# Kernel tuning notes

Hardware: AMD Instinct MI355X
Metric: run time of the kernel (lower is better)

Reference implementation:

```python
import jax, jax.numpy as jnp
import numpy as np

N = 10000
E = 160000
IN_DIM = 256
PROJ_DIM = 512
HIDDEN = 512
OUT_DIM = 512
HEADS1, HEADS2, HEADS3 = 4, 4, 1
NEG_SLOPE = 0.2  # PyG GATConv default


def gat_conv(x, edge_index, W, att_src, att_dst, bias, heads, out_c, concat):
    """PyG GATConv (eval mode), with self-loops already appended to edge_index.
    x: [N, F_in]; W: [F_in, heads*out_c]; att_src/att_dst: [heads, out_c]; bias: [heads*out_c] or [out_c]."""
    n = x.shape[0]
    h = (x @ W).reshape(n, heads, out_c)            # [N, H, C]
    a_src = jnp.einsum('nhc,hc->nh', h, att_src)     # [N, H]
    a_dst = jnp.einsum('nhc,hc->nh', h, att_dst)     # [N, H]
    src, dst = edge_index[0], edge_index[1]
    e = jax.nn.leaky_relu(a_src[src] + a_dst[dst], NEG_SLOPE)  # [E, H]
    # segment softmax over incoming edges per destination node
    e_max = jax.ops.segment_max(e, dst, num_segments=n)
    e_exp = jnp.exp(e - e_max[dst])
    denom = jax.ops.segment_sum(e_exp, dst, num_segments=n)
    alpha = e_exp / denom[dst]                       # [E, H]
    msg = alpha[:, :, None] * h[src]                 # [E, H, C]
    out = jax.ops.segment_sum(msg, dst, num_segments=n)  # [N, H, C]
    out = out.reshape(n, heads * out_c) if concat else out.mean(axis=1)
    return out + bias


def setup_inputs() -> dict:
    key = jax.random.key(0)
    ks = jax.random.split(key, 16)
    g = 0.1
    inp = {
        'x': jax.random.normal(ks[0], (N, IN_DIM), dtype=jnp.float32),
        'edge_index': jax.random.randint(ks[1], (2, E), 0, N, dtype=jnp.int64),
        'proj_W': jax.random.normal(ks[2], (IN_DIM, PROJ_DIM), dtype=jnp.float32) * g,
        'proj_b': jnp.zeros((PROJ_DIM,), dtype=jnp.float32),
        'W1': jax.random.normal(ks[3], (PROJ_DIM, HEADS1 * HIDDEN), dtype=jnp.float32) * g,
        'as1': jax.random.normal(ks[4], (HEADS1, HIDDEN), dtype=jnp.float32) * g,
        'ad1': jax.random.normal(ks[5], (HEADS1, HIDDEN), dtype=jnp.float32) * g,
        'b1': jnp.zeros((HEADS1 * HIDDEN,), dtype=jnp.float32),
        'W2': jax.random.normal(ks[6], (HEADS1 * HIDDEN, HEADS2 * HIDDEN), dtype=jnp.float32) * g * 0.5,
        'as2': jax.random.normal(ks[7], (HEADS2, HIDDEN), dtype=jnp.float32) * g,
        'ad2': jax.random.normal(ks[8], (HEADS2, HIDDEN), dtype=jnp.float32) * g,
        'b2': jnp.zeros((HEADS2 * HIDDEN,), dtype=jnp.float32),
        'W3': jax.random.normal(ks[9], (HEADS2 * HIDDEN, HEADS3 * OUT_DIM), dtype=jnp.float32) * g * 0.5,
        'as3': jax.random.normal(ks[10], (HEADS3, OUT_DIM), dtype=jnp.float32) * g,
        'ad3': jax.random.normal(ks[11], (HEADS3, OUT_DIM), dtype=jnp.float32) * g,
        'b3': jnp.zeros((OUT_DIM,), dtype=jnp.float32),
    }
    return inp


def reference(x, edge_index, proj_W, proj_b, W1, as1, ad1, b1, W2, as2, ad2, b2, W3, as3, ad3, b3):
    # append self-loops once (PyG GATConv add_self_loops=True)
    loops = jnp.arange(N, dtype=edge_index.dtype)
    ei = jnp.concatenate([edge_index, jnp.stack([loops, loops])], axis=1)
    h = x @ proj_W + proj_b                                   # [N, 512]
    h = jax.nn.elu(gat_conv(h, ei, W1, as1, ad1, b1, HEADS1, HIDDEN, True))
    h = jax.nn.elu(gat_conv(h, ei, W2, as2, ad2, b2, HEADS2, HIDDEN, True))
    return gat_conv(h, ei, W3, as3, ad3, b3, HEADS3, OUT_DIM, False)  # [N, 512]
```

## Files before the change

kernel.cpp:

```cpp
#include <hip/hip_runtime.h>
#include <hip/hip_bf16.h>


#define LB(x) __launch_bounds__(x)

typedef unsigned short u16;
typedef unsigned int u32;
typedef __attribute__((ext_vector_type(8))) short short8;
typedef __attribute__((ext_vector_type(8))) short bf16x8;
typedef __attribute__((ext_vector_type(8))) _Float16 f16x8;
typedef __attribute__((ext_vector_type(4))) float f32x4;

__device__ __forceinline__ float b2f(u16 u) {
    union { float f; u32 u; } x;
    x.u = ((u32)u) << 16;
    return x.f;
}
__device__ __forceinline__ u16 f2b(float f) {
    u32 u = __float_as_uint(f);
    u = (u + 0x7FFFu + ((u >> 16) & 1u)) >> 16;
    return (u16)u;
}
__device__ __forceinline__ u16 f2h(float f) {
    union { _Float16 h; u16 u; } x;
    x.h = (_Float16)f;
    return x.u;
}
__device__ __forceinline__ float h2f(u16 u) {
    union { _Float16 h; u16 u; } x;
    x.u = u;
    return (float)x.h;
}
__device__ __forceinline__ void lds_cp16(const void* g, void* l) {
    __builtin_amdgcn_global_load_lds(
        (const __attribute__((address_space(1))) unsigned int*)g,
        (__attribute__((address_space(3))) unsigned int*)l, 16, 0, 0);
}

__global__ void k_deg(const int* __restrict__ ei, int E, int Np, int* __restrict__ deg) {
    int e = blockIdx.x * blockDim.x + threadIdx.x;
    if (e >= E + Np) return;
    int dst = (e < E) ? ei[E + e] : (e - E);
    atomicAdd(&deg[dst], 1);
}

__global__ LB(256) void k_s1(const int* __restrict__ deg, int* __restrict__ row_ptr,
                             int* __restrict__ bsum, int n) {
    __shared__ int sh[256];
    int b = blockIdx.x, t = threadIdx.x;
    int i = b * 256 + t;
    int v = (i < n) ? deg[i] : 0;
    sh[t] = v;
    __syncthreads();
    #pragma unroll
    for (int off = 1; off < 256; off <<= 1) {
        int add = (t >= off) ? sh[t - off] : 0;
        __syncthreads();
        sh[t] += add;
        __syncthreads();
    }
    if (i < n) row_ptr[i + 1] = sh[t];
    if (t == 255) bsum[b] = sh[255];
}

__global__ LB(64) void k_s2(int* __restrict__ bsum, int* __restrict__ boff, int nb) {
    __shared__ int sh[64];
    int t = threadIdx.x;
    sh[t] = (t < nb) ? bsum[t] : 0;
    __syncthreads();
    #pragma unroll
    for (int off = 1; off < 64; off <<= 1) {
        int add = (t >= off) ? sh[t - off] : 0;
        __syncthreads();
        sh[t] += add;
        __syncthreads();
    }
    if (t < nb) boff[t] = (t == 0) ? 0 : sh[t - 1];
}

__global__ LB(256) void k_s3(const int* __restrict__ deg, int* __restrict__ row_ptr,
                             const int* __restrict__ boff, int* __restrict__ cursor, int n) {
    int b = blockIdx.x, t = threadIdx.x;
    int i = b * 256 + t;
    if (i == 0) row_ptr[0] = 0;
    if (i < n) {
        int inc = row_ptr[i + 1] + boff[b];
        row_ptr[i + 1] = inc;
        cursor[i] = inc - deg[i];
    }
}

__global__ void k_fill(const int* __restrict__ ei, int E, int Np,
                       int* __restrict__ cursor, int* __restrict__ col_src) {
    int e = blockIdx.x * blockDim.x + threadIdx.x;
    if (e >= E + Np) return;
    int src, dst;
    if (e < E) { src = ei[e]; dst = ei[E + e]; }
    else       { src = dst = e - E; }
    int pos = atomicAdd(&cursor[dst], 1);
    col_src[pos] = src;
}

__global__ void k_pack(const float* __restrict__ in, u16* __restrict__ hi,
                       u16* __restrict__ lo, int n4) {
    int i = blockIdx.x * blockDim.x + threadIdx.x;
    if (i >= n4) return;
    float4 v = ((const float4*)in)[i];
    ushort4 h, l;
    h.x = f2b(v.x); l.x = f2b(v.x - b2f(h.x));
    h.y = f2b(v.y); l.y = f2b(v.y - b2f(h.y));
    h.z = f2b(v.z); l.z = f2b(v.z - b2f(h.z));
    h.w = f2b(v.w); l.w = f2b(v.w - b2f(h.w));
    ((ushort4*)hi)[i] = h;
    ((ushort4*)lo)[i] = l;
}

template<bool F16>
__global__ LB(256) void k_wt_pack(const float* __restrict__ W, u16* __restrict__ Whi,
                                  u16* __restrict__ Wlo, int K, int Nn) {
    __shared__ float sh[32][33];
    int n0 = blockIdx.x * 32, k0 = blockIdx.y * 32;
    int c = threadIdx.x & 31, r0 = threadIdx.x >> 5;
    #pragma unroll
    for (int r = r0; r < 32; r += 8)
        sh[r][c] = W[(size_t)(k0 + r) * Nn + n0 + c];
    __syncthreads();
    #pragma unroll
    for (int r = r0; r < 32; r += 8) {
        float v = sh[c][r];
        if (F16) {
            u16 hi = f2h(v);
            Whi[(size_t)(n0 + r) * K + k0 + c] = hi;
            Wlo[(size_t)(n0 + r) * K + k0 + c] = f2h(v - h2f(hi));
        } else {
            u16 hi = f2b(v);
            Whi[(size_t)(n0 + r) * K + k0 + c] = hi;
            Wlo[(size_t)(n0 + r) * K + k0 + c] = f2b(v - b2f(hi));
        }
    }
}

template<int NFR, int PREC, int OUTMODE, bool ATT>
__global__ LB(256) void k_gemm_pl(const u16* __restrict__ Ahi, const u16* __restrict__ Alo,
                                  const u16* __restrict__ Bhi, const u16* __restrict__ Blo,
                                  const float* __restrict__ bias,
                                  u16* __restrict__ Chi, u16* __restrict__ Clo,
                                  u16* __restrict__ Cf16,
                                  const float* __restrict__ att_s, const float* __restrict__ att_d,
                                  float* __restrict__ a_src, float* __restrict__ a_dst,
                                  int HH, int M, int K, int Nn) {
    constexpr int BN = NFR * 32;
    constexpr int ALO_SZ = (PREC == 0) ? 128 * 32 : 8;
    __shared__ u16 AsHi[128 * 32];
    __shared__ u16 AsLo[ALO_SZ];
    __shared__ u16 BsHi[BN * 32], BsLo[BN * 32];
    const int tid  = threadIdx.x;
    const int lane = tid & 63;
    const int w    = tid >> 6;
    const int wr   = w >> 1;
    const int wc   = w & 1;
    const int row0 = blockIdx.y * 128;
    const int col0 = blockIdx.x * BN;
    const int ln15 = lane & 15;
    const int lq   = lane >> 4;

    f32x4 acc[4][NFR];
    #pragma unroll
    for (int m = 0; m < 4; ++m)
        #pragma unroll
        for (int n = 0; n < NFR; ++n) acc[m][n] = (f32x4){0.f, 0.f, 0.f, 0.f};

    for (int k0 = 0; k0 < K; k0 += 32) {
        #pragma unroll
        for (int i = 0; i < 2; ++i) {
            int c = i * 256 + tid;
            int r  = 2 * (c >> 3) + (((c >> 2) ^ (c >> 4)) & 1);
            int kc = (c & 3) ^ (r & 3);
            int gra = row0 + r; if (gra >= M) gra = M - 1;
            size_t ga = (size_t)gra * K + k0 + kc * 8;
            lds_cp16(Ahi + ga, (char*)AsHi + c * 16);
            if (PREC == 0) lds_cp16(Alo + ga, (char*)AsLo + c * 16);
        }
        #pragma unroll
        for (int i = 0; i < NFR / 2; ++i) {
            int c = i * 256 + tid;
            int r  = 2 * (c >> 3) + (((c >> 2) ^ (c >> 4)) & 1);
            int kc = (c & 3) ^ (r & 3);
            size_t gb = (size_t)(col0 + r) * K + k0 + kc * 8;
            lds_cp16(Bhi + gb, (char*)BsHi + c * 16);
            lds_cp16(Blo + gb, (char*)BsLo + c * 16);
        }
        __syncthreads();
        if (PREC == 0) {
            bf16x8 ah[4], al[4], bh[NFR], bl[NFR];
            #pragma unroll
            for (int m = 0; m < 4; ++m) {
                int row = wr * 64 + m * 16 + ln15;
                int byo = (row * 64 + lq * 16) ^ ((row & 7) << 4);
                ah[m] = *(const bf16x8*)((const char*)AsHi + byo);
                al[m] = *(const bf16x8*)((const char*)AsLo + byo);
            }
            #pragma unroll
            for (int n = 0; n < NFR; ++n) {
                int row = wc * (NFR * 16) + n * 16 + ln15;
                int byo = (row * 64 + lq * 16) ^ ((row & 7) << 4);
                bh[n] = *(const bf16x8*)((const char*)BsHi + byo);
                bl[n] = *(const bf16x8*)((const char*)BsLo + byo);
            }
            #pragma unroll
            for (int m = 0; m < 4; ++m)
                #pragma unroll
                for (int n = 0; n < NFR; ++n) {
                    acc[m][n] = __builtin_amdgcn_mfma_f32_16x16x32_bf16(al[m], bh[n], acc[m][n], 0, 0, 0);
                    acc[m][n] = __builtin_amdgcn_mfma_f32_16x16x32_bf16(ah[m], bl[n], acc[m][n], 0, 0, 0);
                    acc[m][n] = __builtin_amdgcn_mfma_f32_16x16x32_bf16(ah[m], bh[n], acc[m][n], 0, 0, 0);
                }
        } else {
            f16x8 a[4], bh[NFR], bl[NFR];
            #pragma unroll
            for (int m = 0; m < 4; ++m) {
                int row = wr * 64 + m * 16 + ln15;
                int byo = (row * 64 + lq * 16) ^ ((row & 7) << 4);
                a[m] = *(const f16x8*)((const char*)AsHi + byo);
            }
            #pragma unroll
            for (int n = 0; n < NFR; ++n) {
                int row = wc * (NFR * 16) + n * 16 + ln15;
                int byo = (row * 64 + lq * 16) ^ ((row & 7) << 4);
                bh[n] = *(const f16x8*)((const char*)BsHi + byo);
                bl[n] = *(const f16x8*)((const char*)BsLo + byo);
            }
            #pragma unroll
            for (int m = 0; m < 4; ++m)
                #pragma unroll
                for (int n = 0; n < NFR; ++n) {
                    acc[m][n] = __builtin_amdgcn_mfma_f32_16x16x32_f16(a[m], bl[n], acc[m][n], 0, 0, 0);
                    acc[m][n] = __builtin_amdgcn_mfma_f32_16x16x32_f16(a[m], bh[n], acc[m][n], 0, 0, 0);
                }
        }
        __syncthreads();
    }

    #pragma unroll
    for (int m = 0; m < 4; ++m) {
        #pragma unroll
        for (int n = 0; n < NFR; ++n) {
            int gc = col0 + wc * (NFR * 16) + n * 16 + ln15;
            float badd = (OUTMODE == 0 && bias) ? bias[gc] : 0.f;
            #pragma unroll
            for (int j = 0; j < 4; ++j) {
                int gr = row0 + wr * 64 + m * 16 + lq * 4 + j;
                if (gr < M) {
                    float v = acc[m][n][j] + badd;
                    size_t o = (size_t)gr * Nn + gc;
                    if (OUTMODE == 0) {
                        u16 hi = f2b(v);
                        Chi[o] = hi;
                        Clo[o] = f2b(v - b2f(hi));
                    } else {
                        Cf16[o] = f2h(v);
                    }
                }
            }
        }
    }

    if (ATT) {
        float atts[NFR], attd[NFR];
        #pragma unroll
        for (int n = 0; n < NFR; ++n) {
            int gc = col0 + wc * (NFR * 16) + n * 16 + ln15;
            atts[n] = att_s[gc];
            attd[n] = att_d[gc];
        }
        const int head = (col0 + wc * (NFR * 16)) >> 9;
        #pragma unroll
        for (int m = 0; m < 4; ++m) {
            #pragma unroll
            for (int j = 0; j < 4; ++j) {
                int gr = row0 + wr * 64 + m * 16 + lq * 4 + j;
                float s1 = 0.f, s2 = 0.f;
                #pragma unroll
                for (int n = 0; n < NFR; ++n) {
                    float v = acc[m][n][j];
                    s1 = fmaf(v, atts[n], s1);
                    s2 = fmaf(v, attd[n], s2);
                }
                #pragma unroll
                for (int off = 1; off < 16; off <<= 1) {
                    s1 += __shfl_xor(s1, off);
                    s2 += __shfl_xor(s2, off);
                }
                if (ln15 == 0 && gr < M) {
                    atomicAdd(&a_src[gr * HH + head], s1);
                    atomicAdd(&a_dst[gr * HH + head], s2);
                }
            }
        }
    }
}

template<int HH>
__global__ LB(64) void k_softmax(const int* __restrict__ row_ptr, const int* __restrict__ col_src,
                                 const float* __restrict__ a_src, const float* __restrict__ a_dst,
                                 float* __restrict__ alpha) {
    int d = blockIdx.x;
    int t = threadIdx.x;
    int s = row_ptr[d], eend = row_ptr[d + 1];
    int cnt = eend - s;
    float adh[HH];
    #pragma unroll
    for (int h = 0; h < HH; ++h) adh[h] = a_dst[d * HH + h];

    if (cnt <= 64) {
        bool act = t < cnt;
        float av[HH];
        #pragma unroll
        for (int h = 0; h < HH; ++h) av[h] = 0.f;
        if (act) {
            int src = col_src[s + t];
            if (HH == 4) {
                float4 q = ((const float4*)a_src)[src];
                av[0] = q.x; av[1] = q.y; av[2] = q.z; av[3] = q.w;
            } else {
                av[0] = a_src[src];
            }
        }
        float v[HH], m[HH], sum[HH];
        #pragma unroll
        for (int h = 0; h < HH; ++h) {
            float x = av[h] + adh[h];
            x = (x > 0.f) ? x : 0.2f * x;
            v[h] = act ? x : -1e30f;
            m[h] = v[h];
        }
        #pragma unroll
        for (int off = 32; off; off >>= 1)
            #pragma unroll
            for (int h = 0; h < HH; ++h) m[h] = fmaxf(m[h], __shfl_xor(m[h], off));
        #pragma unroll
        for (int h = 0; h < HH; ++h) {
            float e = act ? __expf(v[h] - m[h]) : 0.f;
            v[h] = e;
            sum[h] = e;
        }
        #pragma unroll
        for (int off = 32; off; off >>= 1)
            #pragma unroll
            for (int h = 0; h < HH; ++h) sum[h] += __shfl_xor(sum[h], off);
        if (act) {
            if (HH == 4) {
                float4 o;
                o.x = v[0] / sum[0]; o.y = v[1] / sum[1];
                o.z = v[2] / sum[2]; o.w = v[3] / sum[3];
                ((float4*)alpha)[s + t] = o;
            } else {
                alpha[s + t] = v[0] / sum[0];
            }
        }
        return;
    }

    for (int h = 0; h < HH; ++h) {
        float m = -1e30f;
        for (int e = s + t; e < eend; e += 64) {
            float x = a_src[col_src[e] * HH + h] + adh[h];
            x = (x > 0.f) ? x : 0.2f * x;
            m = fmaxf(m, x);
        }
        #pragma unroll
        for (int off = 32; off; off >>= 1) m = fmaxf(m, __shfl_xor(m, off));
        float sum = 0.f;
        for (int e = s + t; e < eend; e += 64) {
            float x = a_src[col_src[e] * HH + h] + adh[h];
            x = (x > 0.f) ? x : 0.2f * x;
            sum += __expf(x - m);
        }
        #pragma unroll
        for (int off = 32; off; off >>= 1) sum += __shfl_xor(sum, off);
        float inv = 1.0f / sum;
        for (int e = s + t; e < eend; e += 64) {
            float x = a_src[col_src[e] * HH + h] + adh[h];
            x = (x > 0.f) ? x : 0.2f * x;
            alpha[e * HH + h] = __expf(x - m) * inv;
        }
    }
}

template <int OMODE, bool ELU_>
__global__ LB(256) void k_agg(const int* __restrict__ row_ptr, const int* __restrict__ col_src,
                              const float* __restrict__ alpha, const u16* __restrict__ hf,
                              const float* __restrict__ bias,
                              u16* __restrict__ Oh, float* __restrict__ Of, int H, int C) {
    int d = blockIdx.x;
    int tid = threadIdx.x;
    int F = H * C;
    int o = tid * 8;
    int h0 = o / C;
    float acc[8];
    #pragma unroll
    for (int j = 0; j < 8; ++j) acc[j] = 0.f;
    int s = row_ptr[d], eend = row_ptr[d + 1];

    short8 v; float a;
    if (s < eend) {
        int src = col_src[s];
        a = alpha[s * H + h0];
        v = *(const short8*)(hf + (size_t)src * F + o);
    }
    for (int e = s; e < eend; ++e) {
        short8 w_; float an;
        bool more = (e + 1 < eend);
        if (more) {
            int srcn = col_src[e + 1];
            an = alpha[(e + 1) * H + h0];
            w_ = *(const short8*)(hf + (size_t)srcn * F + o);
        }
        #pragma unroll
        for (int j = 0; j < 8; ++j)
            acc[j] = fmaf(a, h2f((u16)v[j]), acc[j]);
        if (more) { a = an; v = w_; }
    }

    #pragma unroll
    for (int j = 0; j < 8; ++j) {
        acc[j] += bias[o + j];
        if (ELU_) acc[j] = (acc[j] > 0.f) ? acc[j] : __expf(acc[j]) - 1.f;
    }
    if (OMODE == 0) {
        short8 r;
        #pragma unroll
        for (int j = 0; j < 8; ++j) r[j] = (short)f2h(acc[j]);
        *(short8*)(Oh + (size_t)d * F + o) = r;
    } else {
        float* po = Of + (size_t)d * F + o;
        #pragma unroll
        for (int j4 = 0; j4 < 2; ++j4) {
            float4 r;
            r.x = acc[j4 * 4 + 0]; r.y = acc[j4 * 4 + 1];
            r.z = acc[j4 * 4 + 2]; r.w = acc[j4 * 4 + 3];
            *(float4*)&po[j4 * 4] = r;
        }
    }
}

extern "C" void kernel_launch(void* const* d_in, const int* in_sizes, int n_in,
                              void* d_out, int out_size, void* d_ws, size_t ws_size,
                              hipStream_t stream) {
    const float* x      = (const float*)d_in[0];
    const int*   ei     = (const int*)d_in[1];
    const float* proj_W = (const float*)d_in[2];
    const float* proj_b = (const float*)d_in[3];
    const float* W1  = (const float*)d_in[4];
    const float* as1 = (const float*)d_in[5];
    const float* ad1 = (const float*)d_in[6];
    const float* b1  = (const float*)d_in[7];
    const float* W2  = (const float*)d_in[8];
    const float* as2 = (const float*)d_in[9];
    const float* ad2 = (const float*)d_in[10];
    const float* b2  = (const float*)d_in[11];
    const float* W3  = (const float*)d_in[12];
    const float* as3 = (const float*)d_in[13];
    const float* ad3 = (const float*)d_in[14];
    const float* b3  = (const float*)d_in[15];

    const int N  = in_sizes[0] / 256;
    const int E  = in_sizes[1] / 2;
    const int Ep = E + N;
    const int NB = (N + 255) / 256;

    size_t off = 0;
    auto alloc = [&](size_t bytes) -> void* {
        void* p = (char*)d_ws + off;
        off += (bytes + 255) & ~(size_t)255;
        return p;
    };
    u16* bufX    = (u16*)alloc((size_t)N * 2048 * 2);
    u16* bufY    = (u16*)alloc((size_t)N * 2048 * 2);
    u16* proj_hi = (u16*)alloc((size_t)N * 512 * 2);
    u16* proj_lo = (u16*)alloc((size_t)N * 512 * 2);
    u16* xb_hi   = (u16*)alloc((size_t)N * 256 * 2);
    u16* xb_lo   = (u16*)alloc((size_t)N * 256 * 2);
    float* att_z   = (float*)alloc((size_t)N * 18 * 4);
    float* alpha   = (float*)alloc((size_t)Ep * 4 * 4);
    int*   deg     = (int*)alloc((size_t)N * 4);
    int*   cursor  = (int*)alloc((size_t)N * 4);
    int*   row_ptr = (int*)alloc((size_t)(N + 1) * 4);
    int*   col_src = (int*)alloc((size_t)Ep * 4);
    int*   bsum    = (int*)alloc((size_t)NB * 4);
    int*   boff    = (int*)alloc((size_t)NB * 4);
    (void)ws_size;

    float* a_src1 = att_z;
    float* a_dst1 = att_z + (size_t)N * 4;
    float* a_src2 = att_z + (size_t)N * 8;
    float* a_dst2 = att_z + (size_t)N * 12;
    float* a_src3 = att_z + (size_t)N * 16;
    float* a_dst3 = att_z + (size_t)N * 17;

    u16* whi = (u16*)d_out;
    u16* wlo = (u16*)d_out + (size_t)2048 * 2048;

    hipMemsetAsync(deg, 0, (size_t)N * 4, stream);
    hipMemsetAsync(att_z, 0, (size_t)N * 18 * 4, stream);
    int eb = (Ep + 255) / 256;
    k_deg<<<eb, 256, 0, stream>>>(ei, E, N, deg);
    k_s1<<<NB, 256, 0, stream>>>(deg, row_ptr, bsum, N);
    k_s2<<<1, 64, 0, stream>>>(bsum, boff, NB);
    k_s3<<<NB, 256, 0, stream>>>(deg, row_ptr, boff, cursor, N);
    k_fill<<<eb, 256, 0, stream>>>(ei, E, N, cursor, col_src);

    const int MB1 = (N + 127) / 128;

    k_pack<<<(N * 256 / 4 + 255) / 256, 256, 0, stream>>>(x, xb_hi, xb_lo, N * 256 / 4);

    k_wt_pack<false><<<dim3(512 / 32, 256 / 32), 256, 0, stream>>>(proj_W, whi, wlo, 256, 512);
    k_gemm_pl<2, 0, 0, false><<<dim3(512 / 64, MB1), 256, 0, stream>>>(
        xb_hi, xb_lo, whi, wlo, proj_b, proj_hi, proj_lo, nullptr,
        nullptr, nullptr, nullptr, nullptr, 0, N, 256, 512);

    k_wt_pack<false><<<dim3(2048 / 32, 512 / 32), 256, 0, stream>>>(W1, whi, wlo, 512, 2048);
    k_gemm_pl<4, 0, 2, true><<<dim3(2048 / 128, MB1), 256, 0, stream>>>(
        proj_hi, proj_lo, whi, wlo, nullptr, nullptr, nullptr, bufX,
        as1, ad1, a_src1, a_dst1, 4, N, 512, 2048);
    k_softmax<4><<<N, 64, 0, stream>>>(row_ptr, col_src, a_src1, a_dst1, alpha);
    k_agg<0, true><<<N, 256, 0, stream>>>(row_ptr, col_src, alpha, bufX,
                                          b1, bufY, nullptr, 4, 512);

    k_wt_pack<true><<<dim3(2048 / 32, 2048 / 32), 256, 0, stream>>>(W2, whi, wlo, 2048, 2048);
    k_gemm_pl<4, 1, 2, true><<<dim3(2048 / 128, MB1), 256, 0, stream>>>(
        bufY, nullptr, whi, wlo, nullptr, nullptr, nullptr, bufX,
        as2, ad2, a_src2, a_dst2, 4, N, 2048, 2048);
    k_softmax<4><<<N, 64, 0, stream>>>(row_ptr, col_src, a_src2, a_dst2, alpha);
    k_agg<0, true><<<N, 256, 0, stream>>>(row_ptr, col_src, alpha, bufX,
                                          b2, bufY, nullptr, 4, 512);

    k_wt_pack<true><<<dim3(512 / 32, 2048 / 32), 256, 0, stream>>>(W3, whi, wlo, 2048, 512);
    k_gemm_pl<2, 1, 2, true><<<dim3(512 / 64, MB1), 256, 0, stream>>>(
        bufY, nullptr, whi, wlo, nullptr, nullptr, nullptr, bufX,
        as3, ad3, a_src3, a_dst3, 1, N, 2048, 512);
    k_softmax<1><<<N, 64, 0, stream>>>(row_ptr, col_src, a_src3, a_dst3, alpha);
    k_agg<1, false><<<N, 64, 0, stream>>>(row_ptr, col_src, alpha, bufX,
                                          b3, nullptr, (float*)d_out, 1, 512);
}
```

Measured before the change: 760.4 us.

## Fold input projection into first GAT weight matrix to skip projection GEMM

Precomputes the fused weight W1^T·proj_W^T (2048x256) and a folded bias proj_b·W1, so layer 1's GEMM reads the packed input x directly with K=256 instead of K=512. This removes the N×256×512 projection GEMM and halves the K dimension of the first layer GEMM, at the cost of a small weight-only GEMM and a bias-fold kernel per call. The bias is now added in the f16 output path and in the attention-logit reduction, and precision of the fused weights relies on hi/lo split products.

Measured after the change: 759.0 us. About the same (-0.2%).

```diff
diff --git a/kernel.cpp b/kernel.cpp
--- a/kernel.cpp
+++ b/kernel.cpp
@@ -138,6 +138,21 @@
             Wlo[(size_t)(n0 + r) * K + k0 + c] = f2b(v - b2f(hi));
         }
     }
+}
+
+__global__ LB(64) void k_bfold(const float* __restrict__ pb,
+                               const u16* __restrict__ w1t_hi, const u16* __restrict__ w1t_lo,
+                               float* __restrict__ bfold, int K) {
+    int n = blockIdx.x;
+    int lane = threadIdx.x;
+    float s = 0.f;
+    for (int k = lane; k < K; k += 64) {
+        float w = b2f(w1t_hi[(size_t)n * K + k]) + b2f(w1t_lo[(size_t)n * K + k]);
+        s = fmaf(pb[k], w, s);
+    }
+    #pragma unroll
+    for (int off = 32; off; off >>= 1) s += __shfl_xor(s, off);
+    if (lane == 0) bfold[n] = s;
 }
 
 template<int NFR, int PREC, int OUTMODE, bool ATT>
@@ -246,7 +261,7 @@
         #pragma unroll
         for (int n = 0; n < NFR; ++n) {
             int gc = col0 + wc * (NFR * 16) + n * 16 + ln15;
-            float badd = (OUTMODE == 0 && bias) ? bias[gc] : 0.f;
+            float badd = bias ? bias[gc] : 0.f;
             #pragma unroll
             for (int j = 0; j < 4; ++j) {
                 int gr = row0 + wr * 64 + m * 16 + lq * 4 + j;
@@ -266,12 +281,13 @@
     }
 
     if (ATT) {
-        float atts[NFR], attd[NFR];
+        float atts[NFR], attd[NFR], bb[NFR];
         #pragma unroll
         for (int n = 0; n < NFR; ++n) {
             int gc = col0 + wc * (NFR * 16) + n * 16 + ln15;
             atts[n] = att_s[gc];
             attd[n] = att_d[gc];
+            bb[n]   = bias ? bias[gc] : 0.f;
         }
         const int head = (col0 + wc * (NFR * 16)) >> 9;
         #pragma unroll
@@ -282,7 +298,7 @@
                 float s1 = 0.f, s2 = 0.f;
                 #pragma unroll
                 for (int n = 0; n < NFR; ++n) {
-                    float v = acc[m][n][j];
+                    float v = acc[m][n][j] + bb[n];
                     s1 = fmaf(v, atts[n], s1);
                     s2 = fmaf(v, attd[n], s2);
                 }
@@ -477,10 +493,13 @@
     };
     u16* bufX    = (u16*)alloc((size_t)N * 2048 * 2);
     u16* bufY    = (u16*)alloc((size_t)N * 2048 * 2);
-    u16* proj_hi = (u16*)alloc((size_t)N * 512 * 2);
-    u16* proj_lo = (u16*)alloc((size_t)N * 512 * 2);
     u16* xb_hi   = (u16*)alloc((size_t)N * 256 * 2);
     u16* xb_lo   = (u16*)alloc((size_t)N * 256 * 2);
+    u16* pw_hi   = (u16*)alloc((size_t)256 * 512 * 2);
+    u16* pw_lo   = (u16*)alloc((size_t)256 * 512 * 2);
+    u16* wf_hi   = (u16*)alloc((size_t)2048 * 256 * 2);
+    u16* wf_lo   = (u16*)alloc((size_t)2048 * 256 * 2);
+    float* bfold   = (float*)alloc((size_t)2048 * 4);
     float* att_z   = (float*)alloc((size_t)N * 18 * 4);
     float* alpha   = (float*)alloc((size_t)Ep * 4 * 4);
     int*   deg     = (int*)alloc((size_t)N * 4);
@@ -513,16 +532,17 @@
     const int MB1 = (N + 127) / 128;
 
     k_pack<<<(N * 256 / 4 + 255) / 256, 256, 0, stream>>>(x, xb_hi, xb_lo, N * 256 / 4);
-
-    k_wt_pack<false><<<dim3(512 / 32, 256 / 32), 256, 0, stream>>>(proj_W, whi, wlo, 256, 512);
-    k_gemm_pl<2, 0, 0, false><<<dim3(512 / 64, MB1), 256, 0, stream>>>(
-        xb_hi, xb_lo, whi, wlo, proj_b, proj_hi, proj_lo, nullptr,
-        nullptr, nullptr, nullptr, nullptr, 0, N, 256, 512);
+    k_pack<<<(256 * 512 / 4 + 255) / 256, 256, 0, stream>>>(proj_W, pw_hi, pw_lo, 256 * 512 / 4);
 
     k_wt_pack<false><<<dim3(2048 / 32, 512 / 32), 256, 0, stream>>>(W1, whi, wlo, 512, 2048);
+    k_bfold<<<2048, 64, 0, stream>>>(proj_b, whi, wlo, bfold, 512);
+    k_gemm_pl<2, 0, 0, false><<<dim3(256 / 64, 2048 / 128), 256, 0, stream>>>(
+        whi, wlo, pw_hi, pw_lo, nullptr, wf_hi, wf_lo, nullptr,
+        nullptr, nullptr, nullptr, nullptr, 0, 2048, 512, 256);
+
     k_gemm_pl<4, 0, 2, true><<<dim3(2048 / 128, MB1), 256, 0, stream>>>(
-        proj_hi, proj_lo, whi, wlo, nullptr, nullptr, nullptr, bufX,
-        as1, ad1, a_src1, a_dst1, 4, N, 512, 2048);
+        xb_hi, xb_lo, wf_hi, wf_lo, bfold, nullptr, nullptr, bufX,
+        as1, ad1, a_src1, a_dst1, 4, N, 256, 2048);
     k_softmax<4><<<N, 64, 0, stream>>>(row_ptr, col_src, a_src1, a_dst1, alpha);
     k_agg<0, true><<<N, 256, 0, stream>>>(row_ptr, col_src, alpha, bufX,
                                           b1, bufY, nullptr, 4, 512);
```
